# Performance work log

Hardware: AMD Instinct MI355X
Metric: run time of the kernel (lower is better)

Reference implementation:

```python
import jax, jax.numpy as jnp
import numpy as np

B, T, C = 8, 4096, 1024


def setup_inputs() -> dict:
    key = jax.random.key(0)
    ks = jax.random.split(key, 5)
    scales = (jnp.arange(C, dtype=jnp.float32) / C).reshape(1, 1, C)
    return {
        "x": jax.random.normal(ks[0], (B, T, C), dtype=jnp.float32),
        "time_decay": scales,
        "time_first": scales,
        "time_mix_k": scales,
        "time_mix_v": scales,
        "time_mix_r": scales,
        "Wk": jax.random.normal(ks[1], (C, C), dtype=jnp.float32) / np.sqrt(C),
        "Wv": jax.random.normal(ks[2], (C, C), dtype=jnp.float32) / np.sqrt(C),
        "Wr": jax.random.normal(ks[3], (C, C), dtype=jnp.float32) / np.sqrt(C),
        "Wo": jax.random.normal(ks[4], (C, C), dtype=jnp.float32) / np.sqrt(C),
    }


def _wkv(w_decay, u_first, k, v):
    # w_decay, u_first: [C]; k, v: [B, T, C]
    w = -jnp.exp(w_decay)  # per original: w = -w.exp()
    u = u_first
    kt = jnp.transpose(k, (1, 0, 2))  # [T, B, C]
    vt = jnp.transpose(v, (1, 0, 2))
    a0 = jnp.zeros((k.shape[0], k.shape[2]), dtype=k.dtype)
    b0 = jnp.zeros_like(a0)
    p0 = jnp.full_like(a0, -1e38)  # running max exponent

    def step(carry, kv):
        a, b, p = carry
        k_t, v_t = kv
        # output at t (includes bonus u for current token)
        q = jnp.maximum(p, u + k_t)
        e1 = jnp.exp(p - q)
        e2 = jnp.exp(u + k_t - q)
        y = (e1 * a + e2 * v_t) / (e1 * b + e2)
        # state update with decay w
        q2 = jnp.maximum(p + w, k_t)
        f1 = jnp.exp(p + w - q2)
        f2 = jnp.exp(k_t - q2)
        return (f1 * a + f2 * v_t, f1 * b + f2, q2), y

    _, y = jax.lax.scan(step, (a0, b0, p0), (kt, vt))
    return jnp.transpose(y, (1, 0, 2))  # [B, T, C]


def reference(x, time_decay, time_first, time_mix_k, time_mix_v, time_mix_r, Wk, Wv, Wr, Wo):
    # time shift: prev token, zero-padded at t=0 (ZeroPad2d((0,0,1,-1)))
    x_prev = jnp.pad(x, ((0, 0), (1, 0), (0, 0)))[:, :-1]
    # torch.lerp(a, b, w) = a + w*(b-a)
    xk = x_prev + time_mix_k * (x - x_prev)
    xv = x_prev + time_mix_v * (x - x_prev)
    xr = x_prev + time_mix_r * (x - x_prev)
    k = jnp.einsum('btc,dc->btd', xk, Wk)
    v = jnp.einsum('btc,dc->btd', xv, Wv)
    sr = jax.nn.sigmoid(jnp.einsum('btc,dc->btd', xr, Wr))
    wkv = _wkv(time_decay.reshape(-1), time_first.reshape(-1), k, v)
    return jnp.einsum('btc,dc->btd', sr * wkv, Wo)
```

## Files before the change

kernel.cpp:

```cpp
#include <hip/hip_runtime.h>
#include <hip/hip_bf16.h>
#include <hip/hip_fp16.h>


#define BH 8
#define TT 4096
#define CC 1024
#define NCH 64
#define CHL (TT / NCH)

typedef _Float16       f16x8  __attribute__((ext_vector_type(8)));
typedef float          f32x4  __attribute__((ext_vector_type(4)));
typedef unsigned short ushort_t;

__device__ __forceinline__ ushort_t f2h_u(float f) {
  return __half_as_ushort(__float2half(f));
}

#define GLOAD_LDS16(g, l)                                                     \
  __builtin_amdgcn_global_load_lds(                                           \
      (const __attribute__((address_space(1))) unsigned int*)(g),             \
      (__attribute__((address_space(3))) unsigned int*)(l), 16, 0, 0)

#define BARRIER() do { asm volatile("" ::: "memory");                        \
                       __builtin_amdgcn_s_barrier();                          \
                       asm volatile("" ::: "memory"); } while (0)

#define LGKM0() do { asm volatile("s_waitcnt lgkmcnt(0)" ::: "memory");      \
                     __builtin_amdgcn_sched_barrier(0); } while (0)

#define WAITV(n) do { asm volatile("s_waitcnt vmcnt(" #n ")" ::: "memory");  \
                      __builtin_amdgcn_sched_barrier(0); } while (0)

__global__ __launch_bounds__(256)
void split_w(const float* __restrict__ W0, const float* __restrict__ W1,
             const float* __restrict__ W2, const float* __restrict__ W3,
             ushort_t* __restrict__ out)
{
  int idx = blockIdx.x * 256 + threadIdx.x;
  int w = idx >> 20;
  int e = idx & (CC * CC - 1);
  const float* src = (w == 0) ? W0 : (w == 1) ? W1 : (w == 2) ? W2 : W3;
  out[(size_t)w * CC * CC + e] = f2h_u(src[e]);
}

__global__ __launch_bounds__(256)
void lerp_one(const float* __restrict__ x, const float* __restrict__ mix,
              ushort_t* __restrict__ oh)
{
  const int idx = blockIdx.x * 256 + threadIdx.x;
  const int m = idx >> 8;
  const int c = (idx & 255) * 4;
  const size_t e = (size_t)m * CC + c;
  float4 xv = *(const float4*)(x + e);
  float4 xp = make_float4(0.f, 0.f, 0.f, 0.f);
  if ((m & (TT - 1)) != 0) xp = *(const float4*)(x + e - CC);
  float4 mx = *(const float4*)(mix + c);
  float a0 = xp.x + mx.x * (xv.x - xp.x);
  float a1 = xp.y + mx.y * (xv.y - xp.y);
  float a2 = xp.z + mx.z * (xv.z - xp.z);
  float a3 = xp.w + mx.w * (xv.w - xp.w);
  *(ushort4*)(oh + e) = make_ushort4(f2h_u(a0), f2h_u(a1), f2h_u(a2), f2h_u(a3));
}

template<int EPI>
__global__ __launch_bounds__(512)
void gemm_f16(const ushort_t* __restrict__ Ah, const ushort_t* __restrict__ Bh,
              void* __restrict__ Dv)
{
  constexpr int NS = 16;

  __shared__ __align__(16) ushort_t lds[2][2][2][8192];

  const int tid  = threadIdx.x;
  const int wave = tid >> 6, lane = tid & 63;
  const int wm = wave & 1, wn = wave >> 1;
  const int lr = lane & 15, kg = lane >> 4;

  const int bid = blockIdx.x;
  const int swz = (bid & 7) * 64 + (bid >> 3);
  const int m0 = (swz >> 2) * 256;
  const int n0 = (swz & 3) * 256;

  f32x4 acc[8][4] = {};

  auto stage = [&](int s, int h) {
    if (s >= NS) return;
    const int kk = s * 64 + h * 32;
    #pragma unroll
    for (int op = 0; op < 2; ++op) {
      const ushort_t* g0 = op ? Bh : Ah;
      const int r0 = op ? n0 : m0;
      #pragma unroll
      for (int c = 0; c < 2; ++c) {
        const int row = c * 128 + (tid >> 2);
        const int q   = (tid & 3) ^ ((row >> 1) & 3);
        const ushort_t* src = g0 + (size_t)(r0 + row) * CC + kk + q * 8;
        ushort_t* dst = &lds[s & 1][h][op][c * 4096 + wave * 512];
        GLOAD_LDS16(src, dst);
      }
    }
  };
  auto rdA = [&](int b, int h, int fm) -> f16x8 {
    const int row = wm * 128 + fm * 16 + lr;
    const int q   = kg ^ ((row >> 1) & 3);
    return *(const f16x8*)&lds[b][h][0][row * 32 + q * 8];
  };
  auto rdB = [&](int b, int h, int fn) -> f16x8 {
    const int row = wn * 64 + fn * 16 + lr;
    const int q   = kg ^ ((row >> 1) & 3);
    return *(const f16x8*)&lds[b][h][1][row * 32 + q * 8];
  };

  stage(0, 0); stage(0, 1); stage(1, 0); stage(1, 1);
  WAITV(8);
  BARRIER();

  f16x8 Acur[8];
  #pragma unroll
  for (int fm = 0; fm < 8; ++fm) Acur[fm] = rdA(0, 0, fm);

  for (int s = 0; s < NS; ++s) {
    const int b = s & 1;

    f16x8 Bfr[4];
    #pragma unroll
    for (int fn = 0; fn < 4; ++fn) Bfr[fn] = rdB(b, 0, fn);
    f16x8 Anx[8];
    #pragma unroll
    for (int fm = 0; fm < 8; ++fm) Anx[fm] = rdA(b, 1, fm);
    __builtin_amdgcn_s_setprio(1);
    #pragma unroll
    for (int fm = 0; fm < 8; ++fm)
      #pragma unroll
      for (int fn = 0; fn < 4; ++fn)
        acc[fm][fn] = __builtin_amdgcn_mfma_f32_16x16x32_f16(Acur[fm], Bfr[fn], acc[fm][fn], 0, 0, 0);
    __builtin_amdgcn_s_setprio(0);
    LGKM0();
    BARRIER();
    stage(s + 2, 0);
    if (s == NS - 2) { WAITV(4); } else { WAITV(8); }

    f16x8 Bf2[4];
    #pragma unroll
    for (int fn = 0; fn < 4; ++fn) Bf2[fn] = rdB(b, 1, fn);
    #pragma unroll
    for (int fm = 0; fm < 8; ++fm) Acur[fm] = rdA(b ^ 1, 0, fm);
    __builtin_amdgcn_s_setprio(1);
    #pragma unroll
    for (int fm = 0; fm < 8; ++fm)
      #pragma unroll
      for (int fn = 0; fn < 4; ++fn)
        acc[fm][fn] = __builtin_amdgcn_mfma_f32_16x16x32_f16(Anx[fm], Bf2[fn], acc[fm][fn], 0, 0, 0);
    __builtin_amdgcn_s_setprio(0);
    LGKM0();
    BARRIER();
    stage(s + 2, 1);
    if (s == NS - 2)      { WAITV(0); }
    else if (s < NS - 2)  { WAITV(8); }
  }

  float*  Df = (float*)Dv;
  __half* Dh = (__half*)Dv;
  #pragma unroll
  for (int fm = 0; fm < 8; ++fm)
    #pragma unroll
    for (int fn = 0; fn < 4; ++fn) {
      const int col  = n0 + wn * 64 + fn * 16 + lr;
      const int rowb = m0 + wm * 128 + fm * 16 + kg * 4;
      #pragma unroll
      for (int r = 0; r < 4; ++r) {
        if (EPI == 0) Df[(size_t)(rowb + r) * CC + col] = acc[fm][fn][r];
        else          Dh[(size_t)(rowb + r) * CC + col] = __float2half(acc[fm][fn][r]);
      }
    }
}

__global__ __launch_bounds__(256)
void wkv_phase_a(const __half* __restrict__ kb, const __half* __restrict__ vb,
                 const float* __restrict__ decay,
                 float* __restrict__ SA, float* __restrict__ SB, float* __restrict__ SP)
{
  const int idx = blockIdx.x * 256 + threadIdx.x;
  const int c  = idx & (CC - 1);
  const int bc = idx >> 10;
  const int ch = bc & (NCH - 1);
  const int b  = bc >> 6;
  const float w = -__expf(decay[c]);
  float aa = 0.f, bb = 0.f, pp = -1e38f;
  size_t base = ((size_t)b * TT + (size_t)ch * CHL) * CC + c;
  #pragma unroll 4
  for (int t = 0; t < CHL; ++t) {
    const float kt = __half2float(kb[base]);
    const float vt = __half2float(vb[base]);
    const float q2 = fmaxf(pp + w, kt);
    const float f1 = __expf(pp + w - q2);
    const float f2 = __expf(kt - q2);
    aa = f1 * aa + f2 * vt; bb = f1 * bb + f2; pp = q2;
    base += CC;
  }
  SA[idx] = aa; SB[idx] = bb; SP[idx] = pp;
}

__global__ __launch_bounds__(256)
void wkv_combine(float* __restrict__ SA, float* __restrict__ SB, float* __restrict__ SP,
                 const float* __restrict__ decay)
{
  const int idx = blockIdx.x * 256 + threadIdx.x;
  const int c = idx & (CC - 1);
  const int b = idx >> 10;
  const float w  = -__expf(decay[c]);
  const float wL = w * (float)CHL;
  float aa = 0.f, bb = 0.f, pp = -1e38f;
  for (int ch = 0; ch < NCH; ++ch) {
    const size_t s = ((size_t)b * NCH + ch) * CC + c;
    const float la = SA[s], lb = SB[s], lp = SP[s];
    SA[s] = aa; SB[s] = bb; SP[s] = pp;
    const float pw = pp + wL;
    const float q  = fmaxf(pw, lp);
    const float e1 = __expf(pw - q);
    const float e2 = __expf(lp - q);
    aa = e1 * aa + e2 * la; bb = e1 * bb + e2 * lb; pp = q;
  }
}

__global__ __launch_bounds__(256)
void wkv_phase_c(const __half* __restrict__ kb, const __half* __restrict__ vb,
                 const __half* __restrict__ rb, const float* __restrict__ decay,
                 const float* __restrict__ first,
                 const float* __restrict__ SA, const float* __restrict__ SB,
                 const float* __restrict__ SP,
                 ushort_t* __restrict__ yh)
{
  const int idx = blockIdx.x * 256 + threadIdx.x;
  const int c  = idx & (CC - 1);
  const int bc = idx >> 10;
  const int ch = bc & (NCH - 1);
  const int b  = bc >> 6;
  const float w = -__expf(decay[c]);
  const float u = first[c];
  float aa = SA[idx], bb = SB[idx], pp = SP[idx];
  size_t base = ((size_t)b * TT + (size_t)ch * CHL) * CC + c;
  #pragma unroll 4
  for (int t = 0; t < CHL; ++t) {
    const float kt = __half2float(kb[base]);
    const float vt = __half2float(vb[base]);
    const float rt = __half2float(rb[base]);
    const float q  = fmaxf(pp, u + kt);
    const float e1 = __expf(pp - q);
    const float e2 = __expf(u + kt - q);
    const float yv = (e1 * aa + e2 * vt) / (e1 * bb + e2);
    const float sr = 1.f / (1.f + __expf(-rt));
    yh[base] = f2h_u(sr * yv);
    const float q2 = fmaxf(pp + w, kt);
    const float f1 = __expf(pp + w - q2);
    const float f2 = __expf(kt - q2);
    aa = f1 * aa + f2 * vt; bb = f1 * bb + f2; pp = q2;
    base += CC;
  }
}

extern "C" void kernel_launch(void* const* d_in, const int* in_sizes, int n_in,
                              void* d_out, int out_size, void* d_ws, size_t ws_size,
                              hipStream_t stream) {
  const float* x     = (const float*)d_in[0];
  const float* decay = (const float*)d_in[1];
  const float* first = (const float*)d_in[2];
  const float* mk    = (const float*)d_in[3];
  const float* mv    = (const float*)d_in[4];
  const float* mr    = (const float*)d_in[5];
  const float* Wk    = (const float*)d_in[6];
  const float* Wv    = (const float*)d_in[7];
  const float* Wr    = (const float*)d_in[8];
  const float* Wo    = (const float*)d_in[9];
  float* out = (float*)d_out;

  const size_t nbt = (size_t)BH * TT * CC;
  const size_t WS  = (size_t)CC * CC;
  char* p = (char*)d_ws;
  __half*   kbuf = (__half*)  (p);
  __half*   vbuf = (__half*)  (p +  67108864);
  __half*   rbuf = (__half*)  (p + 134217728);
  ushort_t* Asch = (ushort_t*)(p + 201326592);
  ushort_t* Wsp  = (ushort_t*)(p + 268435456);
  float*    SA   = (float*)   (p + 276824064);
  float*    SB   = (float*)   (p + 278921216);
  float*    SP   = (float*)   (p + 281018368);

  dim3 blk(256);
  const dim3 ggrid(512), gblk(512);
  const unsigned lerpg = (unsigned)(nbt / 4 / 256);

  split_w<<<dim3(4 * CC * CC / 256), blk, 0, stream>>>(Wk, Wv, Wr, Wo, Wsp);

  lerp_one<<<lerpg, blk, 0, stream>>>(x, mk, Asch);
  gemm_f16<1><<<ggrid, gblk, 0, stream>>>(Asch, Wsp + 0 * WS, kbuf);
  lerp_one<<<lerpg, blk, 0, stream>>>(x, mv, Asch);
  gemm_f16<1><<<ggrid, gblk, 0, stream>>>(Asch, Wsp + 1 * WS, vbuf);
  lerp_one<<<lerpg, blk, 0, stream>>>(x, mr, Asch);
  gemm_f16<1><<<ggrid, gblk, 0, stream>>>(Asch, Wsp + 2 * WS, rbuf);

  const int nscan = BH * NCH * CC;
  wkv_phase_a<<<dim3(nscan / 256), blk, 0, stream>>>(kbuf, vbuf, decay, SA, SB, SP);
  wkv_combine<<<dim3(BH * CC / 256), blk, 0, stream>>>(SA, SB, SP, decay);
  wkv_phase_c<<<dim3(nscan / 256), blk, 0, stream>>>(kbuf, vbuf, rbuf, decay, first,
                                                     SA, SB, SP, Asch);

  gemm_f16<0><<<ggrid, gblk, 0, stream>>>(Asch, Wsp + 3 * WS, out);
}
```

Measured before the change: 546.5 us.

## Fuse three lerps into one kernel, batch K/V/R GEMMs, stage fp16 epilogue through LDS

Replaces three separate lerp kernels with one that reads x and the previous row once and writes all three mixed inputs. The three projection GEMMs become a single launch with grid z selecting the input and weight. The fp16 epilogue now stages accumulators through LDS so each thread writes 16-byte coalesced rows instead of scattered 2-byte stores. This cuts redundant reads of x and launch count, and improves store efficiency. The cost is a larger workspace (three separate activation buffers) and extra barriers in the epilogue.

```diff
diff --git a/kernel.cpp b/kernel.cpp
--- a/kernel.cpp
+++ b/kernel.cpp
@@ -45,30 +45,40 @@
 }
 
 __global__ __launch_bounds__(256)
-void lerp_one(const float* __restrict__ x, const float* __restrict__ mix,
-              ushort_t* __restrict__ oh)
+void lerp3(const float* __restrict__ x,
+           const float* __restrict__ mk, const float* __restrict__ mv,
+           const float* __restrict__ mr,
+           ushort_t* __restrict__ xk, ushort_t* __restrict__ xv,
+           ushort_t* __restrict__ xr)
 {
   const int idx = blockIdx.x * 256 + threadIdx.x;
   const int m = idx >> 8;
   const int c = (idx & 255) * 4;
   const size_t e = (size_t)m * CC + c;
-  float4 xv = *(const float4*)(x + e);
-  float4 xp = make_float4(0.f, 0.f, 0.f, 0.f);
-  if ((m & (TT - 1)) != 0) xp = *(const float4*)(x + e - CC);
-  float4 mx = *(const float4*)(mix + c);
-  float a0 = xp.x + mx.x * (xv.x - xp.x);
-  float a1 = xp.y + mx.y * (xv.y - xp.y);
-  float a2 = xp.z + mx.z * (xv.z - xp.z);
-  float a3 = xp.w + mx.w * (xv.w - xp.w);
-  *(ushort4*)(oh + e) = make_ushort4(f2h_u(a0), f2h_u(a1), f2h_u(a2), f2h_u(a3));
+  float4 cu = *(const float4*)(x + e);
+  float4 pv = make_float4(0.f, 0.f, 0.f, 0.f);
+  if ((m & (TT - 1)) != 0) pv = *(const float4*)(x + e - CC);
+
+  const float* mixes[3] = {mk, mv, mr};
+  ushort_t* outs[3] = {xk, xv, xr};
+  #pragma unroll
+  for (int z = 0; z < 3; ++z) {
+    float4 mx = *(const float4*)(mixes[z] + c);
+    float a0 = pv.x + mx.x * (cu.x - pv.x);
+    float a1 = pv.y + mx.y * (cu.y - pv.y);
+    float a2 = pv.z + mx.z * (cu.z - pv.z);
+    float a3 = pv.w + mx.w * (cu.w - pv.w);
+    *(ushort4*)(outs[z] + e) = make_ushort4(f2h_u(a0), f2h_u(a1), f2h_u(a2), f2h_u(a3));
+  }
 }
 
 template<int EPI>
 __global__ __launch_bounds__(512)
-void gemm_f16(const ushort_t* __restrict__ Ah, const ushort_t* __restrict__ Bh,
+void gemm_f16(const ushort_t* __restrict__ Ab, const ushort_t* __restrict__ Bb,
               void* __restrict__ Dv)
 {
   constexpr int NS = 16;
+  const size_t nbt = (size_t)BH * TT * CC;
 
   __shared__ __align__(16) ushort_t lds[2][2][2][8192];
 
@@ -76,6 +86,10 @@
   const int wave = tid >> 6, lane = tid & 63;
   const int wm = wave & 1, wn = wave >> 1;
   const int lr = lane & 15, kg = lane >> 4;
+
+  const int z = blockIdx.z;
+  const ushort_t* Ah = Ab + (size_t)z * nbt;
+  const ushort_t* Bh = Bb + (size_t)z * CC * CC;
 
   const int bid = blockIdx.x;
   const int swz = (bid & 7) * 64 + (bid >> 3);
@@ -160,20 +174,41 @@
     else if (s < NS - 2)  { WAITV(8); }
   }
 
-  float*  Df = (float*)Dv;
-  __half* Dh = (__half*)Dv;
-  #pragma unroll
-  for (int fm = 0; fm < 8; ++fm)
-    #pragma unroll
-    for (int fn = 0; fn < 4; ++fn) {
-      const int col  = n0 + wn * 64 + fn * 16 + lr;
-      const int rowb = m0 + wm * 128 + fm * 16 + kg * 4;
-      #pragma unroll
-      for (int r = 0; r < 4; ++r) {
-        if (EPI == 0) Df[(size_t)(rowb + r) * CC + col] = acc[fm][fn][r];
-        else          Dh[(size_t)(rowb + r) * CC + col] = __float2half(acc[fm][fn][r]);
+  if (EPI == 0) {
+    float* Df = (float*)Dv;
+    #pragma unroll
+    for (int fm = 0; fm < 8; ++fm)
+      #pragma unroll
+      for (int fn = 0; fn < 4; ++fn) {
+        const int col  = n0 + wn * 64 + fn * 16 + lr;
+        const int rowb = m0 + wm * 128 + fm * 16 + kg * 4;
+        #pragma unroll
+        for (int r = 0; r < 4; ++r)
+          Df[(size_t)(rowb + r) * CC + col] = acc[fm][fn][r];
       }
+  } else {
+    __half* Dh = (__half*)Dv + (size_t)z * nbt;
+    __half* ep = (__half*)&lds[0][0][0][0];
+    const int rowl = tid >> 4;
+    const int ck   = tid & 15;
+    #pragma unroll
+    for (int s = 0; s < 8; ++s) {
+      __syncthreads();
+      #pragma unroll
+      for (int fn = 0; fn < 4; ++fn)
+        #pragma unroll
+        for (int r = 0; r < 4; ++r)
+          ep[(wm * 16 + kg * 4 + r) * 256 + wn * 64 + fn * 16 + lr] =
+              __float2half(acc[s][fn][r]);
+      __syncthreads();
+      uint4 v0 = *(const uint4*)&ep[rowl * 256 + ck * 16];
+      uint4 v1 = *(const uint4*)&ep[rowl * 256 + ck * 16 + 8];
+      const int grow = m0 + (rowl >> 4) * 128 + s * 16 + (rowl & 15);
+      __half* dst = Dh + (size_t)grow * CC + n0 + ck * 16;
+      *(uint4*)dst = v0;
+      *(uint4*)(dst + 8) = v1;
     }
+  }
 }
 
 __global__ __launch_bounds__(256)
@@ -278,33 +313,31 @@
   const size_t nbt = (size_t)BH * TT * CC;
   const size_t WS  = (size_t)CC * CC;
   char* p = (char*)d_ws;
-  __half*   kbuf = (__half*)  (p);
-  __half*   vbuf = (__half*)  (p +  67108864);
-  __half*   rbuf = (__half*)  (p + 134217728);
-  ushort_t* Asch = (ushort_t*)(p + 201326592);
-  ushort_t* Wsp  = (ushort_t*)(p + 268435456);
-  float*    SA   = (float*)   (p + 276824064);
-  float*    SB   = (float*)   (p + 278921216);
-  float*    SP   = (float*)   (p + 281018368);
+  ushort_t* xk   = (ushort_t*)(p);
+  ushort_t* xv   = (ushort_t*)(p +  67108864);
+  ushort_t* xr   = (ushort_t*)(p + 134217728);
+  __half*   kbuf = (__half*)  (p + 201326592);
+  __half*   vbuf = (__half*)  (p + 268435456);
+  __half*   rbuf = (__half*)  (p + 335544320);
+  ushort_t* Wsp  = (ushort_t*)(p + 402653184);
+  float*    SA   = (float*)   (p + 411041792);
+  float*    SB   = (float*)   (p + 413138944);
+  float*    SP   = (float*)   (p + 415236096);
 
   dim3 blk(256);
-  const dim3 ggrid(512), gblk(512);
+  const dim3 gblk(512);
   const unsigned lerpg = (unsigned)(nbt / 4 / 256);
 
   split_w<<<dim3(4 * CC * CC / 256), blk, 0, stream>>>(Wk, Wv, Wr, Wo, Wsp);
-
-  lerp_one<<<lerpg, blk, 0, stream>>>(x, mk, Asch);
-  gemm_f16<1><<<ggrid, gblk, 0, stream>>>(Asch, Wsp + 0 * WS, kbuf);
-  lerp_one<<<lerpg, blk, 0, stream>>>(x, mv, Asch);
-  gemm_f16<1><<<ggrid, gblk, 0, stream>>>(Asch, Wsp + 1 * WS, vbuf);
-  lerp_one<<<lerpg, blk, 0, stream>>>(x, mr, Asch);
-  gemm_f16<1><<<ggrid, gblk, 0, stream>>>(Asch, Wsp + 2 * WS, rbuf);
+  lerp3<<<dim3(lerpg), blk, 0, stream>>>(x, mk, mv, mr, xk, xv, xr);
+
+  gemm_f16<1><<<dim3(512, 1, 3), gblk, 0, stream>>>(xk, Wsp, (void*)kbuf);
 
   const int nscan = BH * NCH * CC;
   wkv_phase_a<<<dim3(nscan / 256), blk, 0, stream>>>(kbuf, vbuf, decay, SA, SB, SP);
   wkv_combine<<<dim3(BH * CC / 256), blk, 0, stream>>>(SA, SB, SP, decay);
   wkv_phase_c<<<dim3(nscan / 256), blk, 0, stream>>>(kbuf, vbuf, rbuf, decay, first,
-                                                     SA, SB, SP, Asch);
-
-  gemm_f16<0><<<ggrid, gblk, 0, stream>>>(Asch, Wsp + 3 * WS, out);
-}
+                                                     SA, SB, SP, xk);
+
+  gemm_f16<0><<<dim3(512, 1, 1), gblk, 0, stream>>>(xk, Wsp + 3 * WS, (void*)out);
+}
```

New measurement: 499.6 us. 8.6% less time.
